# Kernel tuning notes

Hardware: AMD Instinct MI355X
Metric: run time of the kernel (lower is better)

The kernel has to match this reference:

```python
import math
import jax, jax.numpy as jnp
import numpy as np

B, T, DIN, DH, E, TOPK = 2048, 512, 32, 96, 6, 2


def setup_inputs() -> dict:
    key = jax.random.key(0)
    ks = jax.random.split(key, 20)
    x = jax.random.normal(ks[0], (B, T, DIN), jnp.float32)
    lengths = jax.random.randint(ks[1], (B,), 1, T + 1)
    mask = (jnp.arange(T)[None, :] < lengths[:, None])

    def U(k, shape, fan):
        s = 1.0 / math.sqrt(fan)
        return jax.random.uniform(k, shape, jnp.float32, -s, s)

    # PyTorch LSTM init: U(-1/sqrt(DH), 1/sqrt(DH)); gate order i,f,g,o
    Wih = U(ks[2], (4 * DH, DIN), DH)
    Whh = U(ks[3], (4 * DH, DH), DH)
    bih = U(ks[4], (4 * DH,), DH)
    bhh = U(ks[5], (4 * DH,), DH)
    Wq = U(ks[6], (DH, DH), DH); bq = U(ks[7], (DH,), DH)
    Wk = U(ks[8], (DH, DH), DH); bk = U(ks[9], (DH,), DH)
    Wv = U(ks[10], (DH, DH), DH); bv = U(ks[11], (DH,), DH)
    Wg = U(ks[12], (E, 2 * DH), 2 * DH); bg = U(ks[13], (E,), 2 * DH)
    We1 = U(ks[14], (E, DH, 2 * DH), 2 * DH); be1 = U(ks[15], (E, DH), 2 * DH)
    We2 = U(ks[16], (E, DH), DH); be2 = U(ks[17], (E,), DH)
    return dict(x=x, lengths=lengths, mask=mask, Wih=Wih, Whh=Whh, bih=bih, bhh=bhh,
                Wq=Wq, bq=bq, Wk=Wk, bk=bk, Wv=Wv, bv=bv, Wg=Wg, bg=bg,
                We1=We1, be1=be1, We2=We2, be2=be2)


def _lstm(x, mask, Wih, Whh, bih, bhh):
    # packed-sequence semantics: carry frozen past each sample's length,
    # padded output positions zeroed (like pad_packed_sequence).
    xg = x @ Wih.T + bih  # [B,T,4*DH] precomputed input projection
    dh = Whh.shape[1]

    def step(carry, inp):
        h, c = carry
        xg_t, m_t = inp
        g = xg_t + h @ Whh.T + bhh
        i, f, gg, o = jnp.split(g, 4, axis=-1)
        c_new = jax.nn.sigmoid(f) * c + jax.nn.sigmoid(i) * jnp.tanh(gg)
        h_new = jax.nn.sigmoid(o) * jnp.tanh(c_new)
        m = m_t[:, None]
        h = jnp.where(m, h_new, h)
        c = jnp.where(m, c_new, c)
        return (h, c), jnp.where(m, h_new, 0.0)

    init = (jnp.zeros((x.shape[0], dh), x.dtype), jnp.zeros((x.shape[0], dh), x.dtype))
    (hT, _), H = jax.lax.scan(step, init, (jnp.swapaxes(xg, 0, 1), mask.T))
    return jnp.swapaxes(H, 0, 1), hT  # H:[B,T,DH], hT:[B,DH]


def reference(x, lengths, mask, Wih, Whh, bih, bhh, Wq, bq, Wk, bk, Wv, bv,
              Wg, bg, We1, be1, We2, be2):
    H, hT = _lstm(x, mask, Wih, Whh, bih, bhh)
    Q = hT @ Wq.T + bq                      # [B,DH]
    K = H @ Wk.T + bk                       # [B,T,DH]
    V = H @ Wv.T + bv                       # [B,T,DH]
    logits = jnp.einsum('bd,btd->bt', Q, K) / math.sqrt(K.shape[-1])
    logits = jnp.where(mask, logits, -1e9)
    alpha = jax.nn.softmax(logits, axis=1)  # [B,T]
    ctx = jnp.einsum('bt,btd->bd', alpha, V)
    feats = jnp.concatenate([ctx, hT], axis=-1)  # [B,2*DH]
    gate_logits = feats @ Wg.T + bg              # [B,E]
    topv, topi = jax.lax.top_k(gate_logits, TOPK)
    pi = jax.nn.softmax(topv, axis=-1)           # [B,TOPK]
    # all-expert dense compute (E tiny), then gather selected -> same math as
    # the per-expert masked scatter loop in the torch module (dropout off).
    h1 = jax.nn.relu(jnp.einsum('bf,ehf->beh', feats, We1) + be1[None])  # [B,E,DH]
    outs = jnp.einsum('beh,eh->be', h1, We2) + be2[None]                  # [B,E]
    sel = jnp.take_along_axis(outs, topi, axis=1)                         # [B,TOPK]
    yhat = jnp.sum(pi * sel, axis=-1, keepdims=True)                      # [B,1]
    return yhat, alpha, gate_logits
```

## Files before the change

kernel.cpp:

```cpp
#include <hip/hip_runtime.h>
#include <hip/hip_bf16.h>

#define B_ 2048
#define T_ 512
#define DIN_ 32
#define DH_ 96
#define NG_ 384
#define E_ 6

#define BPB 8
#define HP 104
#define GS 8

typedef __attribute__((ext_vector_type(8))) _Float16 f16x8;
typedef __attribute__((ext_vector_type(4))) float f32x4;

#if defined(__has_builtin)
# if __has_builtin(__builtin_amdgcn_exp2f)
#  define EXP2F(x) __builtin_amdgcn_exp2f(x)
# endif
# if __has_builtin(__builtin_amdgcn_rcpf)
#  define RCPF(x) __builtin_amdgcn_rcpf(x)
# endif
#endif
#ifndef EXP2F
# define EXP2F(x) exp2f(x)
#endif
#ifndef RCPF
# define RCPF(x) (1.0f/(x))
#endif

__device__ __forceinline__ float sigf(float x) {
    return RCPF(1.0f + EXP2F(x * -1.44269504f));
}
__device__ __forceinline__ float tanhf_(float x) {
    return 1.0f - 2.0f * RCPF(1.0f + EXP2F(x * 2.88539008f));
}

__device__ __forceinline__ f16x8 cvt8(float4 a, float4 b) {
    f16x8 r;
    r[0] = (_Float16)a.x; r[1] = (_Float16)a.y; r[2] = (_Float16)a.z; r[3] = (_Float16)a.w;
    r[4] = (_Float16)b.x; r[5] = (_Float16)b.y; r[6] = (_Float16)b.z; r[7] = (_Float16)b.w;
    return r;
}
__device__ __forceinline__ f16x8 cvt8p(const float* p) {
    return cvt8(*(const float4*)p, *(const float4*)(p + 4));
}

__device__ __forceinline__ void lds_barrier() {
    asm volatile("s_waitcnt lgkmcnt(0)\n\ts_barrier" ::: "memory");
}

__global__ __launch_bounds__(512) void sort_zero_kernel(int* __restrict__ bins) {
    bins[threadIdx.x] = 0;
}
__global__ __launch_bounds__(256) void sort_count_kernel(
    const int* __restrict__ lengths, int* __restrict__ bins) {
    const int b = blockIdx.x * 256 + threadIdx.x;
    atomicAdd(&bins[lengths[b] - 1], 1);
}
__global__ __launch_bounds__(512) void sort_scan_kernel(
    const int* __restrict__ bins, int* __restrict__ offs) {
    __shared__ int s[512];
    const int tid = threadIdx.x;
    s[tid] = bins[tid];
    __syncthreads();
    for (int d = 1; d < 512; d <<= 1) {
        int v = (tid >= d) ? s[tid - d] : 0;
        __syncthreads();
        s[tid] += v;
        __syncthreads();
    }
    offs[tid] = s[tid] - bins[tid];
}
__global__ __launch_bounds__(256) void sort_place_kernel(
    const int* __restrict__ lengths, int* __restrict__ offs,
    int* __restrict__ perm) {
    const int b = blockIdx.x * 256 + threadIdx.x;
    const int pos = atomicAdd(&offs[lengths[b] - 1], 1);
    perm[pos] = b;
}

__global__ __launch_bounds__(768, 1) void lstm_kernel(
    const float* __restrict__ x, const int* __restrict__ lengths,
    const int* __restrict__ perm,
    const float* __restrict__ Wih, const float* __restrict__ Whh,
    const float* __restrict__ bih, const float* __restrict__ bhh,
    _Float16* __restrict__ Hout, float* __restrict__ hT)
{
    __shared__ float sgate[NG_ * GS];
    __shared__ _Float16 sh[2][16 * HP];
    __shared__ int sgb[BPB], slen[BPB];

    const int tid  = threadIdx.x;
    const int bb   = blockIdx.x * BPB;
    const int wave = tid >> 6;
    const int lane = tid & 63;
    const int col  = lane & 15;
    const int quad = lane >> 4;

    if (tid < BPB) {
        const int g = perm[bb + tid];
        sgb[tid] = g;
        slen[tid] = lengths[g];
    }
    {
        _Float16* shf = &sh[0][0];
        for (int i = tid; i < 2 * 16 * HP; i += 768) shf[i] = (_Float16)0.f;
    }
    __syncthreads();

    int bmax = slen[0];
#pragma unroll
    for (int i = 1; i < BPB; ++i) bmax = max(bmax, slen[i]);

    int gc[2]; float bias[2];
    f16x8 wh[2][3], wi[2];
#pragma unroll
    for (int j = 0; j < 2; ++j) {
        const int tau = wave * 2 + j;
        const int g = tau / 6, u6 = tau % 6;
        const int gcj = g * DH_ + u6 * 16 + col;
        gc[j] = gcj;
#pragma unroll
        for (int kf = 0; kf < 3; ++kf)
            wh[j][kf] = cvt8p(Whh + gcj * DH_ + kf * 32 + quad * 8);
        wi[j] = cvt8p(Wih + gcj * DIN_ + quad * 8);
        bias[j] = bih[gcj] + bhh[gcj];
    }

    const int eu = tid >> 3;
    const int eb = tid & 7;
    float c1 = 0.f, hk1 = 0.f;
    const int len1 = slen[eb];

    const bool st_act = tid < 384;
    const int sb = tid / 48;
    const int su = (tid % 48) * 2;
    _Float16* Hst = Hout + ((long long)sgb[sb] * T_) * DH_ + su;

    const float* xp = x + ((long long)sgb[col & 7] * T_) * DIN_ + quad * 8;
    float4 xc0 = *(const float4*)xp;
    float4 xc1 = *(const float4*)(xp + 4);

    for (int t = 0; t < bmax; ++t) {
        const int buf = t & 1;

        const _Float16* hrow = &sh[buf][col * HP];
        f16x8 h0 = *(const f16x8*)(hrow + 0  + quad * 8);
        f16x8 h1 = *(const f16x8*)(hrow + 32 + quad * 8);
        f16x8 h2 = *(const f16x8*)(hrow + 64 + quad * 8);

        const float* xpn = (t + 1 < T_) ? (xp + DIN_) : xp;
        float4 xn0 = *(const float4*)xpn;
        float4 xn1 = *(const float4*)(xpn + 4);

        f16x8 xa = cvt8(xc0, xc1);

#pragma unroll
        for (int j = 0; j < 2; ++j) {
            f32x4 a = {bias[j], bias[j], bias[j], bias[j]};
            a = __builtin_amdgcn_mfma_f32_16x16x32_f16(h0, wh[j][0], a, 0, 0, 0);
            a = __builtin_amdgcn_mfma_f32_16x16x32_f16(h1, wh[j][1], a, 0, 0, 0);
            a = __builtin_amdgcn_mfma_f32_16x16x32_f16(h2, wh[j][2], a, 0, 0, 0);
            a = __builtin_amdgcn_mfma_f32_16x16x32_f16(xa, wi[j],    a, 0, 0, 0);
            if (quad < 2)
                *(f32x4*)&sgate[gc[j] * GS + quad * 4] = a;
        }
        lds_barrier();

        if (t > 0 && st_act) {
            unsigned v = *(const unsigned*)&sh[buf][sb * HP + su];
            *(unsigned*)Hst = v;
            Hst += DH_;
        }

        {
            float iv = sgate[(0 * DH_ + eu) * GS + eb];
            float fv = sgate[(1 * DH_ + eu) * GS + eb];
            float gv = sgate[(2 * DH_ + eu) * GS + eb];
            float ov = sgate[(3 * DH_ + eu) * GS + eb];
            float cn = sigf(fv) * c1 + sigf(iv) * tanhf_(gv);
            float hn = sigf(ov) * tanhf_(cn);
            const bool m = t < len1;
            c1  = m ? cn : c1;
            hk1 = m ? hn : hk1;
            sh[buf ^ 1][eb * HP + eu] = (_Float16)hk1;
        }
        lds_barrier();

        xp = xpn; xc0 = xn0; xc1 = xn1;
    }

    if (st_act) {
        unsigned v = *(const unsigned*)&sh[bmax & 1][sb * HP + su];
        *(unsigned*)Hst = v;
    }

    hT[sgb[eb] * DH_ + eu] = hk1;
}

__global__ __launch_bounds__(128) void qk_kernel(
    const float* __restrict__ hT, const float* __restrict__ Wq,
    const float* __restrict__ bq, const float* __restrict__ Wk,
    const float* __restrict__ bk, float* __restrict__ qk_out,
    float* __restrict__ qb_out)
{
    __shared__ float shT[DH_], sQ[DH_];
    const int b = blockIdx.x, tid = threadIdx.x;
    const float scale = 0.10206207262f;
    if (tid < DH_) shT[tid] = hT[b * DH_ + tid];
    __syncthreads();
    if (tid < DH_) {
        float acc = bq[tid];
        const float* wr = Wq + tid * DH_;
        for (int d = 0; d < DH_; d += 4) {
            float4 w4 = *(const float4*)(wr + d);
            acc += w4.x * shT[d] + w4.y * shT[d + 1] + w4.z * shT[d + 2] + w4.w * shT[d + 3];
        }
        sQ[tid] = acc;
    }
    __syncthreads();
    if (tid < DH_) {
        float acc = 0.f;
        for (int j = 0; j < DH_; ++j) acc += Wk[j * DH_ + tid] * sQ[j];
        qk_out[b * DH_ + tid] = acc * scale;
    }
    if (tid == 0) {
        float acc = 0.f;
        for (int d = 0; d < DH_; ++d) acc += sQ[d] * bk[d];
        qb_out[b] = acc * scale;
    }
}

__global__ __launch_bounds__(512) void attn_moe_kernel(
    const _Float16* __restrict__ H, const float* __restrict__ hT,
    const float* __restrict__ qk, const float* __restrict__ qb,
    const int* __restrict__ lengths,
    const float* __restrict__ Wv, const float* __restrict__ bv,
    const float* __restrict__ Wg, const float* __restrict__ bg,
    const float* __restrict__ We1, const float* __restrict__ be1,
    const float* __restrict__ We2, const float* __restrict__ be2,
    float* __restrict__ yhat_out, float* __restrict__ alpha_out,
    float* __restrict__ gl_out)
{
    __shared__ float salpha[T_];
    __shared__ float sqk[DH_];
    __shared__ float spart[4 * DH_];
    __shared__ float sfeats[2 * DH_];
    __shared__ float sh1[2][DH_];
    __shared__ float sred[8], ssum[8];
    __shared__ float sgl[E_];
    __shared__ float spi[2];
    __shared__ int stopi[2];

    const int b = blockIdx.x, tid = threadIdx.x;
    const int len = lengths[b];
    if (tid < DH_) sqk[tid] = qk[b * DH_ + tid];
    const float qbv = qb[b];
    __syncthreads();

    const bool valid = tid < len;
    float l = qbv;
    if (valid) {
        const _Float16* hr = H + ((long long)b * T_ + tid) * DH_;
#pragma unroll
        for (int u = 0; u < DH_; u += 8) {
            f16x8 hv = *(const f16x8*)(hr + u);
            float4 qa = *(const float4*)&sqk[u];
            float4 qc = *(const float4*)&sqk[u + 4];
            l += (float)hv[0] * qa.x + (float)hv[1] * qa.y
               + (float)hv[2] * qa.z + (float)hv[3] * qa.w
               + (float)hv[4] * qc.x + (float)hv[5] * qc.y
               + (float)hv[6] * qc.z + (float)hv[7] * qc.w;
        }
    }
    float lv = valid ? l : -1e30f;

    float m = lv;
    for (int off = 32; off; off >>= 1) m = fmaxf(m, __shfl_xor(m, off));
    if ((tid & 63) == 0) sred[tid >> 6] = m;
    __syncthreads();
    m = sred[0];
#pragma unroll
    for (int i = 1; i < 8; ++i) m = fmaxf(m, sred[i]);

    float e = valid ? EXP2F((l - m) * 1.44269504f) : 0.f;
    float s = e;
    for (int off = 32; off; off >>= 1) s += __shfl_xor(s, off);
    if ((tid & 63) == 0) ssum[tid >> 6] = s;
    __syncthreads();
    s = ssum[0];
#pragma unroll
    for (int i = 1; i < 8; ++i) s += ssum[i];

    const float alpha = e * RCPF(s);
    salpha[tid] = alpha;
    alpha_out[(long long)b * T_ + tid] = alpha;
    __syncthreads();

    if (tid < 4 * DH_) {
        const int s4 = tid / DH_, u = tid - s4 * DH_;
        float acc = 0.f;
        const int t0 = s4 * 128, t1 = min(t0 + 128, len);
        const _Float16* hc = H + ((long long)b * T_) * DH_ + u;
        for (int t = t0; t < t1; ++t)
            acc += salpha[t] * (float)hc[t * DH_];
        spart[s4 * DH_ + u] = acc;
    }
    __syncthreads();
    if (tid < DH_) {
        float craw = spart[tid] + spart[DH_ + tid] + spart[2 * DH_ + tid] + spart[3 * DH_ + tid];
        spart[tid] = craw;
    }
    __syncthreads();
    if (tid < DH_) {
        float acc = bv[tid];
        const float* wr = Wv + tid * DH_;
        for (int u = 0; u < DH_; u += 4) {
            float4 w4 = *(const float4*)(wr + u);
            acc += w4.x * spart[u] + w4.y * spart[u + 1] + w4.z * spart[u + 2] + w4.w * spart[u + 3];
        }
        sfeats[tid] = acc;
        sfeats[DH_ + tid] = hT[b * DH_ + tid];
    }
    __syncthreads();

    if (tid < 192) {
        const int e6 = tid >> 5, cc = tid & 31;
        float p = 0.f;
        const float* wg = Wg + e6 * 2 * DH_;
#pragma unroll
        for (int j = 0; j < 6; ++j) p += wg[cc * 6 + j] * sfeats[cc * 6 + j];
        for (int off = 16; off; off >>= 1) p += __shfl_xor(p, off);
        if (cc == 0) {
            float g = p + bg[e6];
            sgl[e6] = g;
            gl_out[b * E_ + e6] = g;
        }
    }
    __syncthreads();

    if (tid == 0) {
        int i0 = 0; float v0 = sgl[0];
        for (int ee = 1; ee < E_; ++ee) if (sgl[ee] > v0) { v0 = sgl[ee]; i0 = ee; }
        int i1 = -1; float v1 = -1e30f;
        for (int ee = 0; ee < E_; ++ee) {
            if (ee == i0) continue;
            if (sgl[ee] > v1) { v1 = sgl[ee]; i1 = ee; }
        }
        float e1 = EXP2F((v1 - v0) * 1.44269504f);
        float inv = RCPF(1.f + e1);
        spi[0] = inv; spi[1] = e1 * inv;
        stopi[0] = i0; stopi[1] = i1;
    }
    __syncthreads();

    if (tid < 192) {
        const int e2 = tid / DH_, u = tid - e2 * DH_;
        const int ex = stopi[e2];
        float acc = be1[ex * DH_ + u];
        const float* w = We1 + ((long long)ex * DH_ + u) * (2 * DH_);
        for (int f = 0; f < 2 * DH_; f += 4) {
            float4 w4 = *(const float4*)(w + f);
            acc += w4.x * sfeats[f] + w4.y * sfeats[f + 1] + w4.z * sfeats[f + 2] + w4.w * sfeats[f + 3];
        }
        sh1[e2][u] = fmaxf(acc, 0.f);
    }
    __syncthreads();

    if (tid == 0) {
        float outs[2];
#pragma unroll
        for (int e2 = 0; e2 < 2; ++e2) {
            const int ex = stopi[e2];
            float a = be2[ex];
            for (int u = 0; u < DH_; ++u) a += sh1[e2][u] * We2[ex * DH_ + u];
            outs[e2] = a;
        }
        yhat_out[b] = spi[0] * outs[0] + spi[1] * outs[1];
    }
}

extern "C" void kernel_launch(void* const* d_in, const int* in_sizes, int n_in,
                              void* d_out, int out_size, void* d_ws, size_t ws_size,
                              hipStream_t stream) {
    const float* x   = (const float*)d_in[0];
    const int* lengths = (const int*)d_in[1];
    const float* Wih = (const float*)d_in[3];
    const float* Whh = (const float*)d_in[4];
    const float* bih = (const float*)d_in[5];
    const float* bhh = (const float*)d_in[6];
    const float* Wq  = (const float*)d_in[7];
    const float* bq  = (const float*)d_in[8];
    const float* Wk  = (const float*)d_in[9];
    const float* bk  = (const float*)d_in[10];
    const float* Wv  = (const float*)d_in[11];
    const float* bv  = (const float*)d_in[12];
    const float* Wg  = (const float*)d_in[13];
    const float* bg  = (const float*)d_in[14];
    const float* We1 = (const float*)d_in[15];
    const float* be1 = (const float*)d_in[16];
    const float* We2 = (const float*)d_in[17];
    const float* be2 = (const float*)d_in[18];

    float* yhat  = (float*)d_out;
    float* alpha = yhat + B_;
    float* gl    = alpha + (size_t)B_ * T_;

    char* ws = (char*)d_ws;
    _Float16* Hws = (_Float16*)ws;
    float* hTws = (float*)(ws + (size_t)B_ * T_ * DH_ * 2);
    float* qkws = hTws + (size_t)B_ * DH_;
    float* qbws = qkws + (size_t)B_ * DH_;
    int* bins   = (int*)(qbws + B_);
    int* offs   = bins + 512;
    int* perm   = offs + 512;

    sort_zero_kernel<<<dim3(1), dim3(512), 0, stream>>>(bins);
    sort_count_kernel<<<dim3(B_ / 256), dim3(256), 0, stream>>>(lengths, bins);
    sort_scan_kernel<<<dim3(1), dim3(512), 0, stream>>>(bins, offs);
    sort_place_kernel<<<dim3(B_ / 256), dim3(256), 0, stream>>>(lengths, offs, perm);

    lstm_kernel<<<dim3(B_ / BPB), dim3(768), 0, stream>>>(
        x, lengths, perm, Wih, Whh, bih, bhh, Hws, hTws);
    qk_kernel<<<dim3(B_), dim3(128), 0, stream>>>(
        hTws, Wq, bq, Wk, bk, qkws, qbws);
    attn_moe_kernel<<<dim3(B_), dim3(512), 0, stream>>>(
        Hws, hTws, qkws, qbws, lengths, Wv, bv, Wg, bg,
        We1, be1, We2, be2, yhat, alpha, gl);
}
```

Measured before the change: 805.8 us.

## Fuse LSTM gate activations into MFMA epilogue with gate-interleaved weight rows

Weight rows are reordered so each lane's MFMA accumulator holds the i, f, g and o gates for one hidden unit and one batch element. The cell update then runs directly in registers, which removes the shared-memory gate buffer and one block barrier per timestep from the serial recurrence. The block shrinks to 512 threads (8 waves of 3 tiles each). Hidden-state stores past each sequence's length are skipped, which relies on downstream kernels masking those positions. Half of the lanes (batch columns 8-15) do redundant activation work.

```diff
diff --git a/kernel.cpp b/kernel.cpp
--- a/kernel.cpp
+++ b/kernel.cpp
@@ -10,7 +10,8 @@
 
 #define BPB 8
 #define HP 104
-#define GS 8
+#define NW 8
+#define TPW 3
 
 typedef __attribute__((ext_vector_type(8))) _Float16 f16x8;
 typedef __attribute__((ext_vector_type(4))) float f32x4;
@@ -81,14 +82,13 @@
     perm[pos] = b;
 }
 
-__global__ __launch_bounds__(768, 1) void lstm_kernel(
+__global__ __launch_bounds__(512, 1) void lstm_kernel(
     const float* __restrict__ x, const int* __restrict__ lengths,
     const int* __restrict__ perm,
     const float* __restrict__ Wih, const float* __restrict__ Whh,
     const float* __restrict__ bih, const float* __restrict__ bhh,
     _Float16* __restrict__ Hout, float* __restrict__ hT)
 {
-    __shared__ float sgate[NG_ * GS];
     __shared__ _Float16 sh[2][16 * HP];
     __shared__ int sgb[BPB], slen[BPB];
 
@@ -106,7 +106,7 @@
     }
     {
         _Float16* shf = &sh[0][0];
-        for (int i = tid; i < 2 * 16 * HP; i += 768) shf[i] = (_Float16)0.f;
+        for (int i = tid; i < 2 * 16 * HP; i += 512) shf[i] = (_Float16)0.f;
     }
     __syncthreads();
 
@@ -114,29 +114,35 @@
 #pragma unroll
     for (int i = 1; i < BPB; ++i) bmax = max(bmax, slen[i]);
 
-    int gc[2]; float bias[2];
-    f16x8 wh[2][3], wi[2];
-#pragma unroll
-    for (int j = 0; j < 2; ++j) {
-        const int tau = wave * 2 + j;
-        const int g = tau / 6, u6 = tau % 6;
-        const int gcj = g * DH_ + u6 * 16 + col;
-        gc[j] = gcj;
+    f16x8 wh[TPW][3], wi[TPW];
+    f32x4 bias4[TPW];
+    int uu[TPW];
+#pragma unroll
+    for (int j = 0; j < TPW; ++j) {
+        const int tau  = wave * TPW + j;
+        const int gcol = tau * 16 + col;
+        const int ua   = gcol >> 2, ga = gcol & 3;
+        const int wrow = ga * DH_ + ua;
 #pragma unroll
         for (int kf = 0; kf < 3; ++kf)
-            wh[j][kf] = cvt8p(Whh + gcj * DH_ + kf * 32 + quad * 8);
-        wi[j] = cvt8p(Wih + gcj * DIN_ + quad * 8);
-        bias[j] = bih[gcj] + bhh[gcj];
-    }
-
-    const int eu = tid >> 3;
-    const int eb = tid & 7;
-    float c1 = 0.f, hk1 = 0.f;
-    const int len1 = slen[eb];
+            wh[j][kf] = cvt8p(Whh + wrow * DH_ + kf * 32 + quad * 8);
+        wi[j] = cvt8p(Wih + wrow * DIN_ + quad * 8);
+        const int u = tau * 4 + quad;
+        uu[j] = u;
+#pragma unroll
+        for (int r = 0; r < 4; ++r)
+            bias4[j][r] = bih[r * DH_ + u] + bhh[r * DH_ + u];
+    }
+
+    const int lenc = slen[col & 7];
+    float cst[TPW], hk[TPW];
+#pragma unroll
+    for (int j = 0; j < TPW; ++j) { cst[j] = 0.f; hk[j] = 0.f; }
 
     const bool st_act = tid < 384;
-    const int sb = tid / 48;
+    const int sb = (tid / 48) & 7;
     const int su = (tid % 48) * 2;
+    const int len_sb = slen[sb];
     _Float16* Hst = Hout + ((long long)sgb[sb] * T_) * DH_ + su;
 
     const float* xp = x + ((long long)sgb[col & 7] * T_) * DIN_ + quad * 8;
@@ -144,9 +150,9 @@
     float4 xc1 = *(const float4*)(xp + 4);
 
     for (int t = 0; t < bmax; ++t) {
-        const int buf = t & 1;
-
-        const _Float16* hrow = &sh[buf][col * HP];
+        const int cur = t & 1;
+
+        const _Float16* hrow = &sh[cur][col * HP];
         f16x8 h0 = *(const f16x8*)(hrow + 0  + quad * 8);
         f16x8 h1 = *(const f16x8*)(hrow + 32 + quad * 8);
         f16x8 h2 = *(const f16x8*)(hrow + 64 + quad * 8);
@@ -157,47 +163,41 @@
 
         f16x8 xa = cvt8(xc0, xc1);
 
-#pragma unroll
-        for (int j = 0; j < 2; ++j) {
-            f32x4 a = {bias[j], bias[j], bias[j], bias[j]};
-            a = __builtin_amdgcn_mfma_f32_16x16x32_f16(h0, wh[j][0], a, 0, 0, 0);
-            a = __builtin_amdgcn_mfma_f32_16x16x32_f16(h1, wh[j][1], a, 0, 0, 0);
-            a = __builtin_amdgcn_mfma_f32_16x16x32_f16(h2, wh[j][2], a, 0, 0, 0);
-            a = __builtin_amdgcn_mfma_f32_16x16x32_f16(xa, wi[j],    a, 0, 0, 0);
-            if (quad < 2)
-                *(f32x4*)&sgate[gc[j] * GS + quad * 4] = a;
-        }
+        if (t > 0 && st_act && (t - 1) < len_sb) {
+            unsigned v = *(const unsigned*)&sh[cur][sb * HP + su];
+            *(unsigned*)(Hst + (long long)(t - 1) * DH_) = v;
+        }
+
+        const bool m = t < lenc;
+#pragma unroll
+        for (int j = 0; j < TPW; ++j) {
+            f32x4 a = bias4[j];
+            a = __builtin_amdgcn_mfma_f32_16x16x32_f16(wh[j][0], h0, a, 0, 0, 0);
+            a = __builtin_amdgcn_mfma_f32_16x16x32_f16(wh[j][1], h1, a, 0, 0, 0);
+            a = __builtin_amdgcn_mfma_f32_16x16x32_f16(wh[j][2], h2, a, 0, 0, 0);
+            a = __builtin_amdgcn_mfma_f32_16x16x32_f16(wi[j],    xa, a, 0, 0, 0);
+            float cn = sigf(a[1]) * cst[j] + sigf(a[0]) * tanhf_(a[2]);
+            float hn = sigf(a[3]) * tanhf_(cn);
+            if (m) { cst[j] = cn; hk[j] = hn; }
+            if (col < 8)
+                sh[cur ^ 1][col * HP + uu[j]] = (_Float16)hk[j];
+        }
+
         lds_barrier();
 
-        if (t > 0 && st_act) {
-            unsigned v = *(const unsigned*)&sh[buf][sb * HP + su];
-            *(unsigned*)Hst = v;
-            Hst += DH_;
-        }
-
-        {
-            float iv = sgate[(0 * DH_ + eu) * GS + eb];
-            float fv = sgate[(1 * DH_ + eu) * GS + eb];
-            float gv = sgate[(2 * DH_ + eu) * GS + eb];
-            float ov = sgate[(3 * DH_ + eu) * GS + eb];
-            float cn = sigf(fv) * c1 + sigf(iv) * tanhf_(gv);
-            float hn = sigf(ov) * tanhf_(cn);
-            const bool m = t < len1;
-            c1  = m ? cn : c1;
-            hk1 = m ? hn : hk1;
-            sh[buf ^ 1][eb * HP + eu] = (_Float16)hk1;
-        }
-        lds_barrier();
-
         xp = xpn; xc0 = xn0; xc1 = xn1;
     }
 
-    if (st_act) {
+    if (st_act && (bmax - 1) < len_sb) {
         unsigned v = *(const unsigned*)&sh[bmax & 1][sb * HP + su];
-        *(unsigned*)Hst = v;
-    }
-
-    hT[sgb[eb] * DH_ + eu] = hk1;
+        *(unsigned*)(Hst + (long long)(bmax - 1) * DH_) = v;
+    }
+
+    if (col < 8) {
+#pragma unroll
+        for (int j = 0; j < TPW; ++j)
+            hT[sgb[col] * DH_ + uu[j]] = hk[j];
+    }
 }
 
 __global__ __launch_bounds__(128) void qk_kernel(
@@ -422,7 +422,7 @@
     sort_scan_kernel<<<dim3(1), dim3(512), 0, stream>>>(bins, offs);
     sort_place_kernel<<<dim3(B_ / 256), dim3(256), 0, stream>>>(lengths, offs, perm);
 
-    lstm_kernel<<<dim3(B_ / BPB), dim3(768), 0, stream>>>(
+    lstm_kernel<<<dim3(B_ / BPB), dim3(512), 0, stream>>>(
         x, lengths, perm, Wih, Whh, bih, bhh, Hws, hTws);
     qk_kernel<<<dim3(B_), dim3(128), 0, stream>>>(
         hTws, Wq, bq, Wk, bk, qkws, qbws);
```

New measurement: 1.076 ms. 1.34x slower.
